# Kernel optimization log

Measured on AMD Instinct MI355X. Metric: run time of the kernel, lower is better.

The kernel has to match this reference:

```python
import jax, jax.numpy as jnp
import numpy as np

B, T, D, H = 4096, 256, 8, 64  # batch, n_steps, input_dim, hidden_dim


def _init_w(key, shape, fan_in):
    bound = 1.0 / np.sqrt(fan_in)
    return jax.random.uniform(key, shape, jnp.float32, -bound, bound)


def setup_inputs() -> dict:
    key = jax.random.key(0)
    ks = jax.random.split(key, 16)
    Din = D + 1  # features + prev_delta
    return {
        "features": jax.random.normal(ks[0], (B, T, D), jnp.float32),
        # var_selection: Linear(Din->H), ReLU, Linear(H->Din), Softmax
        "W1": _init_w(ks[1], (H, Din), Din), "b1": _init_w(ks[2], (H,), Din),
        "W2": _init_w(ks[3], (Din, H), H), "b2": _init_w(ks[4], (Din,), H),
        # 2-layer LSTM (torch gate order i,f,g,o)
        "Wih0": _init_w(ks[5], (4 * H, Din), H), "Whh0": _init_w(ks[6], (4 * H, H), H),
        "bih0": _init_w(ks[7], (4 * H,), H), "bhh0": _init_w(ks[8], (4 * H,), H),
        "Wih1": _init_w(ks[9], (4 * H, H), H), "Whh1": _init_w(ks[10], (4 * H, H), H),
        "bih1": _init_w(ks[11], (4 * H,), H), "bhh1": _init_w(ks[12], (4 * H,), H),
        # output: Linear(H->1)
        "Wo": _init_w(ks[13], (1, H), H), "bo": _init_w(ks[14], (1,), H),
    }


def _lstm_cell(x, h, c, Wih, Whh, bih, bhh):
    g = x @ Wih.T + bih + h @ Whh.T + bhh
    i, f, gg, o = jnp.split(g, 4, axis=-1)
    c = jax.nn.sigmoid(f) * c + jax.nn.sigmoid(i) * jnp.tanh(gg)
    h = jax.nn.sigmoid(o) * jnp.tanh(c)
    return h, c


def reference(features, W1, b1, W2, b2,
              Wih0, Whh0, bih0, bhh0, Wih1, Whh1, bih1, bhh1, Wo, bo):
    Bn = features.shape[0]
    Hn = Whh0.shape[1]
    dt = features.dtype
    xs = jnp.swapaxes(features, 0, 1)  # (T, B, D) for scan over time
    init = (jnp.zeros((Bn, 1), dt),) + tuple(jnp.zeros((Bn, Hn), dt) for _ in range(4))

    def step(carry, xt):
        prev_delta, h0, c0, h1, c1 = carry
        x = jnp.concatenate([xt, prev_delta], axis=-1)          # (B, D+1)
        w = jax.nn.softmax(jax.nn.relu(x @ W1.T + b1) @ W2.T + b2, axis=-1)
        x = x * w                                               # variable selection
        h0, c0 = _lstm_cell(x, h0, c0, Wih0, Whh0, bih0, bhh0)
        h1, c1 = _lstm_cell(h0, h1, c1, Wih1, Whh1, bih1, bhh1)
        delta = h1 @ Wo.T + bo                                  # (B, 1)
        return (delta, h0, c0, h1, c1), delta[:, 0]

    _, deltas = jax.lax.scan(step, init, xs)  # (T, B)
    return jnp.swapaxes(deltas, 0, 1)         # (B, T)
```

## Files before the change

kernel.cpp:

```cpp
#include <hip/hip_runtime.h>
#include <hip/hip_fp16.h>
#include <math.h>

typedef unsigned int uint;
typedef _Float16 f16x8 __attribute__((ext_vector_type(8)));
typedef __fp16 fp16x2 __attribute__((ext_vector_type(2)));
typedef float f32x4 __attribute__((ext_vector_type(4)));

#define NT 256


#define O_XB   0
#define O_PXH  2048
#define O_H0   6144
#define O_H1   8192
#define O_WP   10240
#define LDS_BYTES 11520

__device__ __forceinline__ float fexp2(float x) { return __builtin_amdgcn_exp2f(x); }
__device__ __forceinline__ float frcp(float x)  { return __builtin_amdgcn_rcpf(x); }

__device__ __forceinline__ uint pkrtz(float lo, float hi) {
    fp16x2 v = __builtin_amdgcn_cvt_pkrtz(lo, hi);
    return __builtin_bit_cast(uint, v);
}
__device__ __forceinline__ uint pack2(float lo, float hi) {
    return ((uint)__half_as_ushort(__float2half_rn(hi)) << 16) |
           (uint)__half_as_ushort(__float2half_rn(lo));
}
__device__ __forceinline__ unsigned short f16b(float x) {
    return __half_as_ushort(__float2half_rn(x));
}
__device__ __forceinline__ f16x8 ldfrag(const uint* p) {
    union { uint4 u; f16x8 h; } c;
    c.u = *(const uint4*)p;
    return c.h;
}
__device__ __forceinline__ uint pkfma_relu(uint acc, uint wv, uint d2) {
    uint r, z = 0u;
    asm("v_pk_fma_f16 %0, %1, %2, %3" : "=v"(r) : "v"(wv), "v"(d2), "v"(acc));
    asm("v_pk_max_f16 %0, %1, %2" : "=v"(r) : "v"(r), "v"(z));
    return r;
}
__device__ __forceinline__ float lstm_out2(const f32x4 a, float& c) {
    float ii = frcp(1.0f + fexp2(a[0]));
    float ff = frcp(1.0f + fexp2(a[1]));
    float gg = fmaf(2.0f, frcp(1.0f + fexp2(a[2])), -1.0f);
    float oo = frcp(1.0f + fexp2(a[3]));
    c = fmaf(ff, c, ii * gg);
    return oo * fmaf(2.0f, frcp(1.0f + fexp2(-2.88539008f * c)), -1.0f);
}
__device__ __forceinline__ float wp_reduce8(const unsigned char* smem, int cb) {
    const float* wp = (const float*)(smem + O_WP) + cb * 20;
    float4 s0 = *(const float4*)(wp);
    float4 s1 = *(const float4*)(wp + 4);
    return ((s0.x + s0.y) + (s0.z + s0.w)) + ((s1.x + s1.y) + (s1.z + s1.w));
}

__global__ __launch_bounds__(1024)
void prep_kernel(const float* __restrict__ W1,  const float* __restrict__ b1,
                 const float* __restrict__ W2,  const float* __restrict__ b2,
                 const float* __restrict__ Wih0, const float* __restrict__ Whh0,
                 const float* __restrict__ bih0, const float* __restrict__ bhh0,
                 const float* __restrict__ Wih1, const float* __restrict__ Whh1,
                 const float* __restrict__ bih1, const float* __restrict__ bhh1,
                 uint* __restrict__ ws)
{
    const int tid = blockIdx.x * 1024 + threadIdx.x;
    float* wsf = (float*)ws;
    const float LOG2E = 1.44269504f;

    if (tid < 12288) {
        int v = tid & 3, l = (tid >> 2) & 63, ts = tid >> 8;
        int s = ts % 3, w = ts / 3;
        int g = l & 3;
        float sc = (g == 2) ? -2.0f * LOG2E : -LOG2E;
        int R = g * 64 + 4 * w + ((l >> 2) & 3);
        int k0 = (l >> 4) * 8 + 2 * v;
        float lo = 0.f, hi = 0.f;
        if (s == 0) {
            if (k0     < 9) lo = Wih0[R * 9 + k0];
            if (k0 + 1 < 9) hi = Wih0[R * 9 + k0 + 1];
            if (k0 == 16)   lo = bih0[R] + bhh0[R];
        } else {
            int kh = 32 * (s - 1) + k0;
            lo = Whh0[R * 64 + kh]; hi = Whh0[R * 64 + kh + 1];
        }
        ws[tid] = pack2(lo * sc, hi * sc);
    } else if (tid < 28672) {
        int idx = tid - 12288;
        int v = idx & 3, l = (idx >> 2) & 63, ts = idx >> 8;
        int s = ts & 3, w = ts >> 2;
        int g = l & 3;
        float sc = (g == 2) ? -2.0f * LOG2E : -LOG2E;
        int R = g * 64 + 4 * w + ((l >> 2) & 3);
        int kt = 32 * s + (l >> 4) * 8 + 2 * v;
        float lo, hi;
        if (kt < 64) { lo = Wih1[R * 64 + kt];      hi = Wih1[R * 64 + kt + 1]; }
        else         { lo = Whh1[R * 64 + kt - 64]; hi = Whh1[R * 64 + kt - 63]; }
        ws[tid] = pack2(lo * sc, hi * sc);
    } else if (tid < 29696) {
        int idx = tid - 28672;
        int v = idx & 3, l = (idx >> 2) & 63, m = idx >> 8;
        int j2 = 16 * m + (l & 15);
        int k0 = (l >> 4) * 8 + 2 * v;
        float lo = (k0 < 9) ? W1[j2 * 9 + k0] : 0.f;
        float hi = 0.f;
        if (k0 + 1 < 9)       hi = W1[j2 * 9 + k0 + 1];
        else if (k0 + 1 == 9) hi = b1[j2];
        if (k0 == 8) lo = 0.f;
        ws[tid] = pack2(lo, hi);
    } else if (tid < 30208) {
        int idx = tid - 29696;
        int v = idx & 3, l = (idx >> 2) & 63, s = idx >> 8;
        int rr = l & 15;
        int k0 = 32 * s + (l >> 4) * 8 + 2 * v;
        float lo = (rr < 9) ? W2[rr * 64 + k0] * LOG2E     : 0.f;
        float hi = (rr < 9) ? W2[rr * 64 + k0 + 1] * LOG2E : 0.f;
        ws[tid] = pack2(lo, hi);
    } else if (tid >= 31232 && tid < 31488) {
        int idx = tid - 31232;
        int r = idx & 3, l = idx >> 2;
        int row = (l >> 4) * 4 + r;
        wsf[tid] = (row < 9) ? b2[row] * LOG2E : -1e30f;
    } else if (tid >= 35584 && tid < 39680) {
        int idx = tid - 35584;
        int r = idx & 3, l = (idx >> 2) & 63, w = idx >> 8;
        float sc = (r == 2) ? -2.0f * LOG2E : -LOG2E;
        int R = r * 64 + 4 * w + (l >> 4);
        wsf[tid] = (bih1[R] + bhh1[R]) * sc;
    }
}

__global__ __launch_bounds__(512, 2)
void tft_main(const float* __restrict__ feat,
              const float* __restrict__ W1,
              const float* __restrict__ Wo, const float* __restrict__ bo,
              const uint* __restrict__ ws,
              float* __restrict__ out)
{
    __shared__ unsigned char smem[LDS_BYTES];
    const int tid  = threadIdx.x;
    const int lane = tid & 63;
    const int w    = tid >> 6;
    const int q    = lane >> 4;
    const int cb   = lane & 15;
    const int b0   = blockIdx.x * 16;
    const int tA   = 2 * w, tB = 2 * w + 1;
    float* wpbuf = (float*)(smem + O_WP);

    {
        uint4 z = {0u, 0u, 0u, 0u};
        #pragma unroll
        for (int i = 0; i < 2; ++i) {
            int idx = tid + i * 512;
            if (idx < LDS_BYTES / 16) ((uint4*)smem)[idx] = z;
        }
    }

    const f16x8 wl0_0A = ldfrag(ws + (tA * 3 + 0) * 256 + lane * 4);
    const f16x8 wl0_1A = ldfrag(ws + (tA * 3 + 1) * 256 + lane * 4);
    const f16x8 wl0_2A = ldfrag(ws + (tA * 3 + 2) * 256 + lane * 4);
    const f16x8 wl0_0B = ldfrag(ws + (tB * 3 + 0) * 256 + lane * 4);
    const f16x8 wl0_1B = ldfrag(ws + (tB * 3 + 1) * 256 + lane * 4);
    const f16x8 wl0_2B = ldfrag(ws + (tB * 3 + 2) * 256 + lane * 4);
    const f16x8 wl1_0A = ldfrag(ws + 12288 + (tA * 4 + 0) * 256 + lane * 4);
    const f16x8 wl1_1A = ldfrag(ws + 12288 + (tA * 4 + 1) * 256 + lane * 4);
    const f16x8 wl1_2A = ldfrag(ws + 12288 + (tA * 4 + 2) * 256 + lane * 4);
    const f16x8 wl1_3A = ldfrag(ws + 12288 + (tA * 4 + 3) * 256 + lane * 4);
    const f16x8 wl1_0B = ldfrag(ws + 12288 + (tB * 4 + 0) * 256 + lane * 4);
    const f16x8 wl1_1B = ldfrag(ws + 12288 + (tB * 4 + 1) * 256 + lane * 4);
    const f16x8 wl1_2B = ldfrag(ws + 12288 + (tB * 4 + 2) * 256 + lane * 4);
    const f16x8 wl1_3B = ldfrag(ws + 12288 + (tB * 4 + 3) * 256 + lane * 4);
    const f16x8 wv2_0 = ldfrag(ws + 29696 + lane * 4);
    const f16x8 wv2_1 = ldfrag(ws + 29696 + 256 + lane * 4);
    f16x8 wv1 = {};
    const float* wsf = (const float*)ws;
    if (w < 4) wv1 = ldfrag(ws + 28672 + w * 256 + lane * 4);
    const float4 b2f   = *(const float4*)(wsf + 31232 + lane * 4);
    const float4 bias1A = *(const float4*)(wsf + 35584 + (tA * 64 + lane) * 4);
    const float4 bias1B = *(const float4*)(wsf + 35584 + (tB * 64 + lane) * 4);
    const float wojA = Wo[8 * w + q];
    const float wojB = Wo[8 * w + 4 + q];
    const float bov  = bo[0];
    uint w8aU[4], w8bU[4];
    #pragma unroll
    for (int e = 0; e < 4; ++e) {
        w8aU[e] = pack2(W1[(q * 8 + 2 * e) * 9 + 8],      W1[(q * 8 + 2 * e + 1) * 9 + 8]);
        w8bU[e] = pack2(W1[(32 + q * 8 + 2 * e) * 9 + 8], W1[(32 + q * 8 + 2 * e + 1) * 9 + 8]);
    }

    float c0A = 0.f, c0B = 0.f, c1A = 0.f, c1B = 0.f;
    f32x4 a0A = {0.f, 0.f, 0.f, 0.f};
    f32x4 a0B = {0.f, 0.f, 0.f, 0.f};
    float4 px   = {0.f, 0.f, 0.f, 0.f};
    float4 dout = {0.f, 0.f, 0.f, 0.f};
    __syncthreads();

    if (tid >= 256) {
        int L = tid - 256, pb = L >> 4, ti = (L >> 1) & 7, ph = L & 1;
        float4 x0 = *(const float4*)(feat + ((size_t)(b0 + pb) * NT + ti) * 8 + 4 * ph);
        uint2 p2; p2.x = pkrtz(x0.x, x0.y); p2.y = pkrtz(x0.z, x0.w);
        *(uint2*)(smem + O_XB + ti * 256 + pb * 16 + ph * 8) = p2;
    }
    if (tid >= 256 && tid < 384) {
        int L = tid - 256, pb = L >> 3, ti = (L >> 1) & 3, ph = L & 1;
        px = *(const float4*)(feat + ((size_t)(b0 + pb) * NT + 8 + ti) * 8 + 4 * ph);
    }
    __syncthreads();

    if (w < 4) {
        union { uint4 u4; f16x8 h; } xb;
        xb.u4 = (uint4){0u, 0u, 0u, 0u};
        if (q == 0)      xb.u4 = *(const uint4*)(smem + O_XB + cb * 16);
        else if (q == 1) xb.u4.x = 0x3C000000u;
        f32x4 acc = {0.f, 0.f, 0.f, 0.f};
        acc = __builtin_amdgcn_mfma_f32_16x16x32_f16(wv1, xb.h, acc, 0, 0, 0);
        uint2 ph; ph.x = pkrtz(acc[0], acc[1]); ph.y = pkrtz(acc[2], acc[3]);
        *(uint2*)(smem + O_PXH + (2 * w + (q >> 1)) * 256 + cb * 16 + (q & 1) * 8) = ph;
    }
    __syncthreads();

    #pragma unroll 1
    for (int tb = 0; tb < NT; tb += 4) {
        #pragma unroll
        for (int u = 0; u < 4; ++u) {
            const int t = tb + u;
            float dlt = 0.f;
            if (t > 0) dlt = wp_reduce8(smem, cb) + bov;
            if (w == 0 && q == 1) {
                if (u == 1)      dout.x = dlt;
                else if (u == 2) dout.y = dlt;
                else if (u == 3) dout.z = dlt;
                else if (t > 0) {
                    dout.w = dlt;
                    *(float4*)(out + (size_t)(b0 + cb) * NT + (t - 4)) = dout;
                }
            }
            f32x4 a1A = {bias1A.x, bias1A.y, bias1A.z, bias1A.w};
            f32x4 a1B = {bias1B.x, bias1B.y, bias1B.z, bias1B.w};
            {
                f16x8 h1a = *(const f16x8*)(smem + O_H1 + lane * 16);
                f16x8 h1b = *(const f16x8*)(smem + O_H1 + 1024 + lane * 16);
                a1A = __builtin_amdgcn_mfma_f32_16x16x32_f16(wl1_2A, h1a, a1A, 0, 0, 0);
                a1B = __builtin_amdgcn_mfma_f32_16x16x32_f16(wl1_2B, h1a, a1B, 0, 0, 0);
                a1A = __builtin_amdgcn_mfma_f32_16x16x32_f16(wl1_3A, h1b, a1A, 0, 0, 0);
                a1B = __builtin_amdgcn_mfma_f32_16x16x32_f16(wl1_3B, h1b, a1B, 0, 0, 0);
            }
            f16x8 hb0, hb1;
            {
                const unsigned char* PX = smem + O_PXH + (t & 1) * 2048;
                uint4 pa = *(const uint4*)(PX + q * 256 + cb * 16);
                uint4 pb = *(const uint4*)(PX + (4 + q) * 256 + cb * 16);
                uint d2 = pkrtz(dlt, dlt);
                union { uint4 u4; f16x8 h; } ca, cbu;
                ca.u4.x  = pkfma_relu(pa.x, w8aU[0], d2);
                ca.u4.y  = pkfma_relu(pa.y, w8aU[1], d2);
                ca.u4.z  = pkfma_relu(pa.z, w8aU[2], d2);
                ca.u4.w  = pkfma_relu(pa.w, w8aU[3], d2);
                cbu.u4.x = pkfma_relu(pb.x, w8bU[0], d2);
                cbu.u4.y = pkfma_relu(pb.y, w8bU[1], d2);
                cbu.u4.z = pkfma_relu(pb.z, w8bU[2], d2);
                cbu.u4.w = pkfma_relu(pb.w, w8bU[3], d2);
                hb0 = ca.h; hb1 = cbu.h;
            }
            {
                f32x4 aA = {b2f.x, b2f.y, b2f.z, b2f.w};
                f32x4 aB = {0.f, 0.f, 0.f, 0.f};
                aA = __builtin_amdgcn_mfma_f32_16x16x32_f16(wv2_0, hb0, aA, 0, 0, 0);
                aB = __builtin_amdgcn_mfma_f32_16x16x32_f16(wv2_1, hb1, aB, 0, 0, 0);
                float e0 = fexp2(aA[0] + aB[0]);
                float e1 = fexp2(aA[1] + aB[1]);
                float e2 = fexp2(aA[2] + aB[2]);
                float e3 = fexp2(aA[3] + aB[3]);
                float sm = (e0 + e1) + (e2 + e3);
                sm += __shfl_xor(sm, 16, 64);
                sm += __shfl_xor(sm, 32, 64);
                float inv = frcp(sm);
                float x0, x1, x2, x3;
                if (q < 2) {
                    uint2 xw2 = *(const uint2*)(smem + O_XB + (t & 7) * 256 + cb * 16 + q * 8);
                    const __half* xh = (const __half*)&xw2;
                    x0 = __half2float(xh[0]); x1 = __half2float(xh[1]);
                    x2 = __half2float(xh[2]); x3 = __half2float(xh[3]);
                } else if (q == 2) { x0 = dlt; x1 = x2 = x3 = 0.f; }
                else               { x0 = x1 = x2 = x3 = 0.f; }
                uint p01 = pkrtz(x0 * e0 * inv, x1 * e1 * inv);
                uint p23 = pkrtz(x2 * e2 * inv, x3 * e3 * inv);
                int srcA = (((2 * q) & 3) << 4) + cb;
                int srcB = (((2 * q + 1) & 3) << 4) + cb;
                uint hA0 = (uint)__shfl((int)p01, srcA, 64);
                uint hA1 = (uint)__shfl((int)p23, srcA, 64);
                uint hB0 = (uint)__shfl((int)p01, srcB, 64);
                uint hB1 = (uint)__shfl((int)p23, srcB, 64);
                union { uint4 u4; f16x8 h; } xs;
                if (q < 2)       xs.u4 = (uint4){hA0, hA1, hB0, hB1};
                else if (q == 2) xs.u4 = (uint4){0x3C00u, 0u, 0u, 0u};
                else             xs.u4 = (uint4){0u, 0u, 0u, 0u};
                a0A = __builtin_amdgcn_mfma_f32_16x16x32_f16(wl0_0A, xs.h, a0A, 0, 0, 0);
                a0B = __builtin_amdgcn_mfma_f32_16x16x32_f16(wl0_0B, xs.h, a0B, 0, 0, 0);
                float hA = lstm_out2(a0A, c0A);
                float hB = lstm_out2(a0B, c0B);
                *(unsigned short*)(smem + O_H0 + w * 256 + cb * 16 + q * 2)     = f16b(hA);
                *(unsigned short*)(smem + O_H0 + w * 256 + cb * 16 + 8 + q * 2) = f16b(hB);
            }
            __syncthreads();

            {
                f16x8 h0a = *(const f16x8*)(smem + O_H0 + lane * 16);
                f16x8 h0b = *(const f16x8*)(smem + O_H0 + 1024 + lane * 16);
                a1A = __builtin_amdgcn_mfma_f32_16x16x32_f16(wl1_0A, h0a, a1A, 0, 0, 0);
                a1B = __builtin_amdgcn_mfma_f32_16x16x32_f16(wl1_0B, h0a, a1B, 0, 0, 0);
                a1A = __builtin_amdgcn_mfma_f32_16x16x32_f16(wl1_1A, h0b, a1A, 0, 0, 0);
                a1B = __builtin_amdgcn_mfma_f32_16x16x32_f16(wl1_1B, h0b, a1B, 0, 0, 0);
                f32x4 anA = {0.f, 0.f, 0.f, 0.f};
                f32x4 anB = {0.f, 0.f, 0.f, 0.f};
                anA = __builtin_amdgcn_mfma_f32_16x16x32_f16(wl0_1A, h0a, anA, 0, 0, 0);
                anB = __builtin_amdgcn_mfma_f32_16x16x32_f16(wl0_1B, h0a, anB, 0, 0, 0);
                anA = __builtin_amdgcn_mfma_f32_16x16x32_f16(wl0_2A, h0b, anA, 0, 0, 0);
                anB = __builtin_amdgcn_mfma_f32_16x16x32_f16(wl0_2B, h0b, anB, 0, 0, 0);
                a0A = anA; a0B = anB;
                float hA = lstm_out2(a1A, c1A);
                float hB = lstm_out2(a1B, c1B);
                *(unsigned short*)(smem + O_H1 + w * 256 + cb * 16 + q * 2)     = f16b(hA);
                *(unsigned short*)(smem + O_H1 + w * 256 + cb * 16 + 8 + q * 2) = f16b(hB);
                float p = fmaf(wojA, hA, wojB * hB);
                p += __shfl_xor(p, 16, 64);
                p += __shfl_xor(p, 32, 64);
                if (q == 0) wpbuf[cb * 20 + w] = p;
            }
            if (w < 4 && t + 1 < NT) {
                union { uint4 u4; f16x8 h; } xb;
                xb.u4 = (uint4){0u, 0u, 0u, 0u};
                if (q == 0)      xb.u4 = *(const uint4*)(smem + O_XB + ((t + 1) & 7) * 256 + cb * 16);
                else if (q == 1) xb.u4.x = 0x3C000000u;
                f32x4 acc = {0.f, 0.f, 0.f, 0.f};
                acc = __builtin_amdgcn_mfma_f32_16x16x32_f16(wv1, xb.h, acc, 0, 0, 0);
                uint2 ph; ph.x = pkrtz(acc[0], acc[1]); ph.y = pkrtz(acc[2], acc[3]);
                *(uint2*)(smem + O_PXH + ((t + 1) & 1) * 2048
                          + (2 * w + (q >> 1)) * 256 + cb * 16 + (q & 1) * 8) = ph;
            }
            if (u == 3 && tid >= 256 && tid < 384) {
                int L = tid - 256, pb = L >> 3, ti = (L >> 1) & 3, ph = L & 1;
                uint2 p2; p2.x = pkrtz(px.x, px.y); p2.y = pkrtz(px.z, px.w);
                *(uint2*)(smem + O_XB + ((tb + 8 + ti) & 7) * 256 + pb * 16 + ph * 8) = p2;
                int tt = tb + 12 + ti;
                if (tt < NT)
                    px = *(const float4*)(feat + ((size_t)(b0 + pb) * NT + tt) * 8 + 4 * ph);
            }
            __syncthreads();
        }
    }

    if (w == 0 && q == 1) {
        dout.w = wp_reduce8(smem, cb) + bov;
        *(float4*)(out + (size_t)(b0 + cb) * NT + (NT - 4)) = dout;
    }
}

extern "C" void kernel_launch(void* const* d_in, const int* in_sizes, int n_in,
                              void* d_out, int out_size, void* d_ws, size_t ws_size,
                              hipStream_t stream) {
    const float* feat = (const float*)d_in[0];
    const float* W1   = (const float*)d_in[1];
    const float* b1   = (const float*)d_in[2];
    const float* W2   = (const float*)d_in[3];
    const float* b2   = (const float*)d_in[4];
    const float* Wih0 = (const float*)d_in[5];
    const float* Whh0 = (const float*)d_in[6];
    const float* bih0 = (const float*)d_in[7];
    const float* bhh0 = (const float*)d_in[8];
    const float* Wih1 = (const float*)d_in[9];
    const float* Whh1 = (const float*)d_in[10];
    const float* bih1 = (const float*)d_in[11];
    const float* bhh1 = (const float*)d_in[12];
    const float* Wo   = (const float*)d_in[13];
    const float* bo   = (const float*)d_in[14];
    uint* ws   = (uint*)d_ws;
    float* out = (float*)d_out;

    hipLaunchKernelGGL(prep_kernel, dim3(40), dim3(1024), 0, stream,
                       W1, b1, W2, b2, Wih0, Whh0, bih0, bhh0,
                       Wih1, Whh1, bih1, bhh1, ws);
    hipLaunchKernelGGL(tft_main, dim3(256), dim3(512), 0, stream,
                       feat, W1, Wo, bo, ws, out);
}
```

Before: 328.5 us.

## Compute output delta via MFMA and shrink layer-0 input MFMA to 16x16x16

```diff
diff --git a/kernel.cpp b/kernel.cpp
--- a/kernel.cpp
+++ b/kernel.cpp
@@ -4,18 +4,20 @@
 
 typedef unsigned int uint;
 typedef _Float16 f16x8 __attribute__((ext_vector_type(8)));
+typedef _Float16 f16x4 __attribute__((ext_vector_type(4)));
 typedef __fp16 fp16x2 __attribute__((ext_vector_type(2)));
 typedef float f32x4 __attribute__((ext_vector_type(4)));
 
 #define NT 256
+
+#define MFMA16(a, b, c) __builtin_amdgcn_mfma_f32_16x16x16f16(a, b, c, 0, 0, 0)
 
 
 #define O_XB   0
 #define O_PXH  2048
 #define O_H0   6144
 #define O_H1   8192
-#define O_WP   10240
-#define LDS_BYTES 11520
+#define LDS_BYTES 10240
 
 __device__ __forceinline__ float fexp2(float x) { return __builtin_amdgcn_exp2f(x); }
 __device__ __forceinline__ float frcp(float x)  { return __builtin_amdgcn_rcpf(x); }
@@ -49,12 +51,6 @@
     float oo = frcp(1.0f + fexp2(a[3]));
     c = fmaf(ff, c, ii * gg);
     return oo * fmaf(2.0f, frcp(1.0f + fexp2(-2.88539008f * c)), -1.0f);
-}
-__device__ __forceinline__ float wp_reduce8(const unsigned char* smem, int cb) {
-    const float* wp = (const float*)(smem + O_WP) + cb * 20;
-    float4 s0 = *(const float4*)(wp);
-    float4 s1 = *(const float4*)(wp + 4);
-    return ((s0.x + s0.y) + (s0.z + s0.w)) + ((s1.x + s1.y) + (s1.z + s1.w));
 }
 
 __global__ __launch_bounds__(1024)
@@ -76,17 +72,20 @@
         int g = l & 3;
         float sc = (g == 2) ? -2.0f * LOG2E : -LOG2E;
         int R = g * 64 + 4 * w + ((l >> 2) & 3);
-        int k0 = (l >> 4) * 8 + 2 * v;
         float lo = 0.f, hi = 0.f;
         if (s == 0) {
-            if (k0     < 9) lo = Wih0[R * 9 + k0];
-            if (k0 + 1 < 9) hi = Wih0[R * 9 + k0 + 1];
-            if (k0 == 16)   lo = bih0[R] + bhh0[R];
+            if (v < 2) {
+                int k0 = (l >> 4) * 4 + 2 * v;
+                if (k0     < 9) lo = Wih0[R * 9 + k0];
+                if (k0 + 1 < 9) hi = Wih0[R * 9 + k0 + 1];
+            }
+            ws[tid] = pack2(lo * sc, hi * sc);
         } else {
+            int k0 = (l >> 4) * 8 + 2 * v;
             int kh = 32 * (s - 1) + k0;
             lo = Whh0[R * 64 + kh]; hi = Whh0[R * 64 + kh + 1];
+            ws[tid] = pack2(lo * sc, hi * sc);
         }
-        ws[tid] = pack2(lo * sc, hi * sc);
     } else if (tid < 28672) {
         int idx = tid - 12288;
         int v = idx & 3, l = (idx >> 2) & 63, ts = idx >> 8;
@@ -123,6 +122,12 @@
         int r = idx & 3, l = idx >> 2;
         int row = (l >> 4) * 4 + r;
         wsf[tid] = (row < 9) ? b2[row] * LOG2E : -1e30f;
+    } else if (tid >= 31488 && tid < 35584) {
+        int idx = tid - 31488;
+        int r = idx & 3, l = (idx >> 2) & 63, w = idx >> 8;
+        float sc = (r == 2) ? -2.0f * LOG2E : -LOG2E;
+        int R = r * 64 + 4 * w + (l >> 4);
+        wsf[tid] = (bih0[R] + bhh0[R]) * sc;
     } else if (tid >= 35584 && tid < 39680) {
         int idx = tid - 35584;
         int r = idx & 3, l = (idx >> 2) & 63, w = idx >> 8;
@@ -147,21 +152,23 @@
     const int cb   = lane & 15;
     const int b0   = blockIdx.x * 16;
     const int tA   = 2 * w, tB = 2 * w + 1;
-    float* wpbuf = (float*)(smem + O_WP);
 
     {
         uint4 z = {0u, 0u, 0u, 0u};
-        #pragma unroll
-        for (int i = 0; i < 2; ++i) {
-            int idx = tid + i * 512;
-            if (idx < LDS_BYTES / 16) ((uint4*)smem)[idx] = z;
-        }
-    }
-
-    const f16x8 wl0_0A = ldfrag(ws + (tA * 3 + 0) * 256 + lane * 4);
+        ((uint4*)smem)[tid] = z;
+        if (tid < LDS_BYTES / 16 - 512) ((uint4*)smem)[512 + tid] = z;
+    }
+
+    f16x4 wl0xA, wl0xB;
+    {
+        union { uint2 u2; f16x4 h; } c;
+        c.u2 = *(const uint2*)(ws + (tA * 3 + 0) * 256 + lane * 4);
+        wl0xA = c.h;
+        c.u2 = *(const uint2*)(ws + (tB * 3 + 0) * 256 + lane * 4);
+        wl0xB = c.h;
+    }
     const f16x8 wl0_1A = ldfrag(ws + (tA * 3 + 1) * 256 + lane * 4);
     const f16x8 wl0_2A = ldfrag(ws + (tA * 3 + 2) * 256 + lane * 4);
-    const f16x8 wl0_0B = ldfrag(ws + (tB * 3 + 0) * 256 + lane * 4);
     const f16x8 wl0_1B = ldfrag(ws + (tB * 3 + 1) * 256 + lane * 4);
     const f16x8 wl0_2B = ldfrag(ws + (tB * 3 + 2) * 256 + lane * 4);
     const f16x8 wl1_0A = ldfrag(ws + 12288 + (tA * 4 + 0) * 256 + lane * 4);
@@ -177,12 +184,26 @@
     f16x8 wv1 = {};
     const float* wsf = (const float*)ws;
     if (w < 4) wv1 = ldfrag(ws + 28672 + w * 256 + lane * 4);
-    const float4 b2f   = *(const float4*)(wsf + 31232 + lane * 4);
+    const float4 b2f    = *(const float4*)(wsf + 31232 + lane * 4);
+    const float4 bias0A = *(const float4*)(wsf + 31488 + (tA * 64 + lane) * 4);
+    const float4 bias0B = *(const float4*)(wsf + 31488 + (tB * 64 + lane) * 4);
     const float4 bias1A = *(const float4*)(wsf + 35584 + (tA * 64 + lane) * 4);
     const float4 bias1B = *(const float4*)(wsf + 35584 + (tB * 64 + lane) * 4);
-    const float wojA = Wo[8 * w + q];
-    const float wojB = Wo[8 * w + 4 + q];
-    const float bov  = bo[0];
+    const float bov = bo[0];
+    f16x8 wdlt0 = {}, wdlt1 = {};
+    if ((lane & 15) == 0) {
+        int kb = (lane >> 4) * 8;
+        union { uint4 u4; f16x8 h; } t0, t1;
+        t0.u4.x = pack2(Wo[kb],     Wo[kb + 1]);
+        t0.u4.y = pack2(Wo[kb + 2], Wo[kb + 3]);
+        t0.u4.z = pack2(Wo[kb + 4], Wo[kb + 5]);
+        t0.u4.w = pack2(Wo[kb + 6], Wo[kb + 7]);
+        t1.u4.x = pack2(Wo[32 + kb],     Wo[32 + kb + 1]);
+        t1.u4.y = pack2(Wo[32 + kb + 2], Wo[32 + kb + 3]);
+        t1.u4.z = pack2(Wo[32 + kb + 4], Wo[32 + kb + 5]);
+        t1.u4.w = pack2(Wo[32 + kb + 6], Wo[32 + kb + 7]);
+        wdlt0 = t0.h; wdlt1 = t1.h;
+    }
     uint w8aU[4], w8bU[4];
     #pragma unroll
     for (int e = 0; e < 4; ++e) {
@@ -191,8 +212,8 @@
     }
 
     float c0A = 0.f, c0B = 0.f, c1A = 0.f, c1B = 0.f;
-    f32x4 a0A = {0.f, 0.f, 0.f, 0.f};
-    f32x4 a0B = {0.f, 0.f, 0.f, 0.f};
+    f32x4 a0A = {bias0A.x, bias0A.y, bias0A.z, bias0A.w};
+    f32x4 a0B = {bias0B.x, bias0B.y, bias0B.z, bias0B.w};
     float4 px   = {0.f, 0.f, 0.f, 0.f};
     float4 dout = {0.f, 0.f, 0.f, 0.f};
     __syncthreads();
@@ -226,8 +247,16 @@
         #pragma unroll
         for (int u = 0; u < 4; ++u) {
             const int t = tb + u;
+            f16x8 h1a = *(const f16x8*)(smem + O_H1 + lane * 16);
+            f16x8 h1b = *(const f16x8*)(smem + O_H1 + 1024 + lane * 16);
             float dlt = 0.f;
-            if (t > 0) dlt = wp_reduce8(smem, cb) + bov;
+            {
+                f32x4 ad = {0.f, 0.f, 0.f, 0.f};
+                ad = __builtin_amdgcn_mfma_f32_16x16x32_f16(wdlt0, h1a, ad, 0, 0, 0);
+                ad = __builtin_amdgcn_mfma_f32_16x16x32_f16(wdlt1, h1b, ad, 0, 0, 0);
+                float dr = __shfl(ad[0], cb, 64);
+                if (t > 0) dlt = dr + bov;
+            }
             if (w == 0 && q == 1) {
                 if (u == 1)      dout.x = dlt;
                 else if (u == 2) dout.y = dlt;
@@ -239,14 +268,10 @@
             }
             f32x4 a1A = {bias1A.x, bias1A.y, bias1A.z, bias1A.w};
             f32x4 a1B = {bias1B.x, bias1B.y, bias1B.z, bias1B.w};
-            {
-                f16x8 h1a = *(const f16x8*)(smem + O_H1 + lane * 16);
-                f16x8 h1b = *(const f16x8*)(smem + O_H1 + 1024 + lane * 16);
-                a1A = __builtin_amdgcn_mfma_f32_16x16x32_f16(wl1_2A, h1a, a1A, 0, 0, 0);
-                a1B = __builtin_amdgcn_mfma_f32_16x16x32_f16(wl1_2B, h1a, a1B, 0, 0, 0);
-                a1A = __builtin_amdgcn_mfma_f32_16x16x32_f16(wl1_3A, h1b, a1A, 0, 0, 0);
-                a1B = __builtin_amdgcn_mfma_f32_16x16x32_f16(wl1_3B, h1b, a1B, 0, 0, 0);
-            }
+            a1A = __builtin_amdgcn_mfma_f32_16x16x32_f16(wl1_2A, h1a, a1A, 0, 0, 0);
+            a1B = __builtin_amdgcn_mfma_f32_16x16x32_f16(wl1_2B, h1a, a1B, 0, 0, 0);
+            a1A = __builtin_amdgcn_mfma_f32_16x16x32_f16(wl1_3A, h1b, a1A, 0, 0, 0);
+            a1B = __builtin_amdgcn_mfma_f32_16x16x32_f16(wl1_3B, h1b, a1B, 0, 0, 0);
             f16x8 hb0, hb1;
             {
                 const unsigned char* PX = smem + O_PXH + (t & 1) * 2048;
@@ -285,20 +310,11 @@
                     x2 = __half2float(xh[2]); x3 = __half2float(xh[3]);
                 } else if (q == 2) { x0 = dlt; x1 = x2 = x3 = 0.f; }
                 else               { x0 = x1 = x2 = x3 = 0.f; }
-                uint p01 = pkrtz(x0 * e0 * inv, x1 * e1 * inv);
-                uint p23 = pkrtz(x2 * e2 * inv, x3 * e3 * inv);
-                int srcA = (((2 * q) & 3) << 4) + cb;
-                int srcB = (((2 * q + 1) & 3) << 4) + cb;
-                uint hA0 = (uint)__shfl((int)p01, srcA, 64);
-                uint hA1 = (uint)__shfl((int)p23, srcA, 64);
-                uint hB0 = (uint)__shfl((int)p01, srcB, 64);
-                uint hB1 = (uint)__shfl((int)p23, srcB, 64);
-                union { uint4 u4; f16x8 h; } xs;
-                if (q < 2)       xs.u4 = (uint4){hA0, hA1, hB0, hB1};
-                else if (q == 2) xs.u4 = (uint4){0x3C00u, 0u, 0u, 0u};
-                else             xs.u4 = (uint4){0u, 0u, 0u, 0u};
-                a0A = __builtin_amdgcn_mfma_f32_16x16x32_f16(wl0_0A, xs.h, a0A, 0, 0, 0);
-                a0B = __builtin_amdgcn_mfma_f32_16x16x32_f16(wl0_0B, xs.h, a0B, 0, 0, 0);
+                union { uint2 u2; f16x4 h; } xs;
+                xs.u2.x = pkrtz(x0 * e0 * inv, x1 * e1 * inv);
+                xs.u2.y = pkrtz(x2 * e2 * inv, x3 * e3 * inv);
+                a0A = MFMA16(wl0xA, xs.h, a0A);
+                a0B = MFMA16(wl0xB, xs.h, a0B);
                 float hA = lstm_out2(a0A, c0A);
                 float hB = lstm_out2(a0B, c0B);
                 *(unsigned short*)(smem + O_H0 + w * 256 + cb * 16 + q * 2)     = f16b(hA);
@@ -313,8 +329,8 @@
                 a1B = __builtin_amdgcn_mfma_f32_16x16x32_f16(wl1_0B, h0a, a1B, 0, 0, 0);
                 a1A = __builtin_amdgcn_mfma_f32_16x16x32_f16(wl1_1A, h0b, a1A, 0, 0, 0);
                 a1B = __builtin_amdgcn_mfma_f32_16x16x32_f16(wl1_1B, h0b, a1B, 0, 0, 0);
-                f32x4 anA = {0.f, 0.f, 0.f, 0.f};
-                f32x4 anB = {0.f, 0.f, 0.f, 0.f};
+                f32x4 anA = {bias0A.x, bias0A.y, bias0A.z, bias0A.w};
+                f32x4 anB = {bias0B.x, bias0B.y, bias0B.z, bias0B.w};
                 anA = __builtin_amdgcn_mfma_f32_16x16x32_f16(wl0_1A, h0a, anA, 0, 0, 0);
                 anB = __builtin_amdgcn_mfma_f32_16x16x32_f16(wl0_1B, h0a, anB, 0, 0, 0);
                 anA = __builtin_amdgcn_mfma_f32_16x16x32_f16(wl0_2A, h0b, anA, 0, 0, 0);
@@ -324,10 +340,6 @@
                 float hB = lstm_out2(a1B, c1B);
                 *(unsigned short*)(smem + O_H1 + w * 256 + cb * 16 + q * 2)     = f16b(hA);
                 *(unsigned short*)(smem + O_H1 + w * 256 + cb * 16 + 8 + q * 2) = f16b(hB);
-                float p = fmaf(wojA, hA, wojB * hB);
-                p += __shfl_xor(p, 16, 64);
-                p += __shfl_xor(p, 32, 64);
-                if (q == 0) wpbuf[cb * 20 + w] = p;
             }
             if (w < 4 && t + 1 < NT) {
                 union { uint4 u4; f16x8 h; } xb;
@@ -352,9 +364,17 @@
         }
     }
 
-    if (w == 0 && q == 1) {
-        dout.w = wp_reduce8(smem, cb) + bov;
-        *(float4*)(out + (size_t)(b0 + cb) * NT + (NT - 4)) = dout;
+    {
+        f16x8 h1a = *(const f16x8*)(smem + O_H1 + lane * 16);
+        f16x8 h1b = *(const f16x8*)(smem + O_H1 + 1024 + lane * 16);
+        f32x4 ad = {0.f, 0.f, 0.f, 0.f};
+        ad = __builtin_amdgcn_mfma_f32_16x16x32_f16(wdlt0, h1a, ad, 0, 0, 0);
+        ad = __builtin_amdgcn_mfma_f32_16x16x32_f16(wdlt1, h1b, ad, 0, 0, 0);
+        float d = __shfl(ad[0], cb, 64) + bov;
+        if (w == 0 && q == 1) {
+            dout.w = d;
+            *(float4*)(out + (size_t)(b0 + cb) * NT + (NT - 4)) = dout;
+        }
     }
 }
 
```

New measurement: 284.0 us. 1.16x faster.
